# Optimization experiments

Hardware: AMD Instinct MI355X
Metric: run time of the kernel (lower is better)

Reference implementation:

```python
import jax, jax.numpy as jnp
import numpy as np

BS = 256          # batch size
N = 1000          # n_step_per_batch
ORDER = 2         # derivative order -> 3 vars (u, u', u'') per step
D = ORDER + 1
STEP_LOGIT = float(np.log(0.001 / 0.999))  # logit(0.001); sigmoid -> 0.001 step size


def mlp(x, w1, b1, w2, b2, w3, b3):
    h = jax.nn.relu(x @ w1 + b1)
    h = jax.nn.relu(h @ w2 + b2)
    return h @ w3 + b3


def build_A(c, h):
    # c: (N, 3) per-step equation coefficients; h: (N-1,) step sizes.
    # Rows: [1 initial-value] + [N equation] + [2*(N-1) Taylor smoothness (d=0,1)].
    R = 1 + N + 2 * (N - 1)
    i = jnp.arange(N)
    j = jnp.arange(N - 1)
    ones = jnp.ones(N - 1, c.dtype)
    rows = jnp.concatenate([
        jnp.array([0]),
        jnp.repeat(1 + i, 3),
        jnp.repeat(1 + N + 2 * j, 4),
        jnp.repeat(2 + N + 2 * j, 3)])
    cols = jnp.concatenate([
        jnp.array([0]),
        (i[:, None] * 3 + jnp.arange(3)).ravel(),
        jnp.stack([3 * j, 3 * j + 1, 3 * j + 2, 3 * (j + 1)], axis=1).ravel(),
        jnp.stack([3 * j + 1, 3 * j + 2, 3 * j + 4], axis=1).ravel()])
    vals = jnp.concatenate([
        jnp.ones(1, c.dtype),
        c.ravel(),
        jnp.stack([-ones, -h, -h * h / 2, ones], axis=1).ravel(),
        jnp.stack([-ones, -h, ones], axis=1).ravel()])
    return jnp.zeros((R, 3 * N), c.dtype).at[rows, cols].add(vals)


def ode_solve(coeffs, rhs, init_iv, steps):
    # coeffs (bs,1,N,3), rhs (bs,N,1), init_iv (bs,1), steps (bs,1,N-1)
    # coeffs/steps are batch-uniform in this model -> single shared system matrix.
    c = coeffs[0, 0]
    h = steps[0, 0]
    A = build_A(c, h)                       # (R, 3N)
    R = A.shape[0]
    b = jnp.zeros((R, BS), A.dtype)
    b = b.at[0].set(init_iv[:, 0]).at[1:1 + N].set(rhs[:, :, 0].T)
    AtA = A.T @ A + 1e-8 * jnp.eye(3 * N, dtype=A.dtype)
    u = jnp.linalg.solve(AtA, A.T @ b)      # (3N, BS) least-squares trajectory
    resid = A @ u - b
    eps = jnp.sqrt(jnp.sum(resid * resid, axis=0))  # (BS,) equation slack norm
    u = u.reshape(N, 3, BS)
    x0 = u[:, 0].T[:, :, None]              # (bs, N, 1)
    x1 = u[:, 1].T[:, :, None]
    x2 = u[:, 2].T[:, :, None]
    return x0, x1, x2, eps, steps


def reference(pin, ptime, pw1, pb1, pw2, pb2, pw3, pb3,
              tw1, tb1, tw2, tb2, tw3, tb3,
              nw1, nb1, nw2, nb2, nw3, nb3, net_iv):
    xi = mlp(pin, pw1, pb1, pw2, pb2, pw3, pb3).reshape(1, 3)
    ts = mlp(ptime, tw1, tb1, tw2, tb2, tw3, tb3).reshape(1, N)
    xi = jnp.tile(xi, (BS, 1))
    ts = jnp.tile(ts, (BS, 1))
    alpha = xi[:, 0:1][:, None, :]                 # (bs,1,1)
    beta = xi[:, 1:2][:, None, :]
    powr = jax.nn.sigmoid(xi[:, 2:3][:, None, :])
    ts = ts[:, None, :]                            # (bs,1,N)
    var = mlp(net_iv.reshape(BS, -1), nw1, nb1, nw2, nb2, nw3, nb3).reshape(BS, 1, N)
    rhs = jnp.abs(alpha * ts + beta * ts ** 2) ** powr * var ** 2 + ts
    rhs = jnp.transpose(rhs, (0, 2, 1))            # (bs, N, 1)
    coeffs = jnp.broadcast_to(jnp.array([0.0, 1.0, 0.0], net_iv.dtype), (BS, 1, N, 3))
    init_iv = var[:, :, 0]                         # (bs, 1)
    steps = jax.nn.sigmoid(jnp.full((BS, 1, N - 1), STEP_LOGIT, net_iv.dtype))
    x0, x1, x2, eps, steps = ode_solve(coeffs, rhs, init_iv, steps)
    x0 = jnp.transpose(x0, (0, 2, 1))              # (bs, 1, N)
    var = jnp.transpose(var, (0, 2, 1))            # (bs, N, 1)
    return (x0, steps, eps, var, ts[:, 0, :], alpha, beta, powr)


def setup_inputs() -> dict:
    key = jax.random.key(0)
    ks = jax.random.split(key, 24)
    f32 = jnp.float32

    def w(k, shape, scale=0.03):
        return (scale * jax.random.normal(k, shape)).astype(f32)

    inp = {
        "pin": w(ks[0], (1, 64), 1.0),
        "ptime": w(ks[1], (1, 64), 1.0),
        "pw1": w(ks[2], (64, 1024)), "pb1": jnp.zeros((1024,), f32),
        "pw2": w(ks[3], (1024, 1024)), "pb2": jnp.zeros((1024,), f32),
        "pw3": w(ks[4], (1024, 3)), "pb3": jnp.zeros((3,), f32),
        "tw1": w(ks[5], (64, 1024)), "tb1": jnp.zeros((1024,), f32),
        "tw2": w(ks[6], (1024, 1024)), "tb2": jnp.zeros((1024,), f32),
        "tw3": w(ks[7], (1024, N)), "tb3": jnp.zeros((N,), f32),
        "nw1": w(ks[8], (N, 1024)), "nb1": jnp.zeros((1024,), f32),
        "nw2": w(ks[9], (1024, 1024)), "nb2": jnp.zeros((1024,), f32),
        "nw3": w(ks[10], (1024, N)), "nb3": jnp.zeros((N,), f32),
        "net_iv": jax.random.normal(ks[11], (BS, N)).astype(f32),
    }
    return inp
```

## Files before the change

### kernel.cpp

```cpp
#include <hip/hip_runtime.h>
#include <math.h>

#define NN 1000
#define NIT 4
#define NKT 16

typedef _Float16 f16;
typedef _Float16 f16x8 __attribute__((ext_vector_type(8)));
typedef _Float16 f16x4 __attribute__((ext_vector_type(4)));
typedef float    f32x4 __attribute__((ext_vector_type(4)));

#define WS_H1P 0
#define WS_H1T 1024
#define WS_H2P 2048
#define WS_H2T 3072
#define WS_TS  4096
#define WS_XI  5120
#define WF_A0  540672
#define WF_H1  802816
#define WF_H2  1064960
#define WF_BT1 1327104
#define WF_BT2 2375680
#define WF_BT3 3424256

#define O_X0    0
#define O_STEP  256000
#define O_EPS   511744
#define O_VAR   512000
#define O_TS    768000
#define O_ALPHA 1024000
#define O_BETA  1024256
#define O_POWR  1024512

__device__ __forceinline__ void conv_bt_body(int idx, const float* __restrict__ W, int K0, int NW,
                                             f16* __restrict__ BT, float (*T)[32][33])
{
    const int tid = threadIdx.x;
    const int tx = tid & 31, ty = tid >> 5;
    const int kt = (idx & 31) * 32, ntile = (idx >> 5) * 32;
    #pragma unroll
    for (int i = 0; i < 4; ++i) {
        int k = kt + ty + i * 8, n = ntile + tx;
        (*T)[ty + i * 8][tx] = (k < K0 && n < NW) ? W[(size_t)k * NW + n] : 0.f;
    }
    __syncthreads();
    #pragma unroll
    for (int i = 0; i < 4; ++i) {
        int n = ntile + ty + i * 8, k = kt + tx;
        BT[(size_t)n * 1024 + k] = (f16)(*T)[tx][ty + i * 8];
    }
}

__device__ __forceinline__ void conv_a_body(int row, const float* __restrict__ in, f16* __restrict__ a0)
{
    const int t = threadIdx.x;
    float4 v = {0.f, 0.f, 0.f, 0.f};
    if (t < 250) v = ((const float4*)(in + row * 1000))[t];
    f16x4 h = {(f16)v.x, (f16)v.y, (f16)v.z, (f16)v.w};
    *(f16x4*)&a0[row * 1024 + t * 4] = h;
}

__device__ __forceinline__ void l1_body(int sub, const float* __restrict__ pin,
    const float* __restrict__ pw1, const float* __restrict__ pb1,
    const float* __restrict__ ptime, const float* __restrict__ tw1, const float* __restrict__ tb1,
    float* __restrict__ ws, float* sin_)
{
    const int tid = threadIdx.x;
    const bool tp = sub >= 4;
    const float* in = tp ? ptime : pin;
    const float* W  = tp ? tw1 : pw1;
    const float* B  = tp ? tb1 : pb1;
    float* outp = ws + (tp ? WS_H1T : WS_H1P);
    const int bxl = sub & 3;
    if (tid < 64) sin_[tid] = in[tid];
    __syncthreads();
    const int u = bxl * 256 + tid;
    float acc = B[u];
    #pragma unroll 16
    for (int k = 0; k < 64; ++k) acc += sin_[k] * W[k * 1024 + u];
    outp[u] = fmaxf(acc, 0.f);
}

__device__ __forceinline__ void l2_body(int lb, const float* __restrict__ pw2, const float* __restrict__ pb2,
    const float* __restrict__ tw2, const float* __restrict__ tb2, float* __restrict__ ws,
    float (*red)[16][17])
{
    const bool tp = lb >= 64;
    const float* h = ws + (tp ? WS_H1T : WS_H1P);
    const float* W = tp ? tw2 : pw2;
    const float* B = tp ? tb2 : pb2;
    float* outp = ws + (tp ? WS_H2T : WS_H2P);
    const int u0 = (lb & 63) * 16;
    const int tid = threadIdx.x, ul = tid & 15, kc = tid >> 4;
    const float* wp = W + u0 + ul;
    float acc = 0.f;
    const int kbase = kc * 64;
    #pragma unroll 8
    for (int k = 0; k < 64; ++k) acc += h[kbase + k] * wp[(size_t)(kbase + k) * 1024];
    (*red)[kc][ul] = acc; __syncthreads();
    for (int s = 8; s; s >>= 1) { if (kc < s) (*red)[kc][ul] += (*red)[kc + s][ul]; __syncthreads(); }
    if (tid < 16) outp[u0 + tid] = fmaxf((*red)[0][tid] + B[u0 + tid], 0.f);
}

__device__ __forceinline__ void l3_body(int lb, const float* __restrict__ pw3, const float* __restrict__ pb3,
    const float* __restrict__ tw3, const float* __restrict__ tb3,
    float* __restrict__ ws, float* __restrict__ out,
    float (*red)[16][17], float* redx)
{
    const int tid = threadIdx.x;
    if (lb == 64) {
        const float* h2p = ws + WS_H2P;
        float p[3] = {0.f, 0.f, 0.f};
        for (int k = tid; k < 1024; k += 256) {
            float h = h2p[k];
            p[0] += h * pw3[k * 3 + 0];
            p[1] += h * pw3[k * 3 + 1];
            p[2] += h * pw3[k * 3 + 2];
        }
        float xi[3];
        #pragma unroll
        for (int j = 0; j < 3; ++j) {
            redx[tid] = p[j]; __syncthreads();
            for (int s = 128; s > 0; s >>= 1) {
                if (tid < s) redx[tid] += redx[tid + s];
                __syncthreads();
            }
            xi[j] = redx[0] + pb3[j];
            __syncthreads();
        }
        float alpha = xi[0], beta = xi[1];
        float powr = 1.f / (1.f + expf(-xi[2]));
        if (tid == 0) { ws[WS_XI + 0] = alpha; ws[WS_XI + 1] = beta; ws[WS_XI + 2] = powr; }
        out[O_ALPHA + tid] = alpha;
        out[O_BETA  + tid] = beta;
        out[O_POWR  + tid] = powr;
    } else {
        const float* h = ws + WS_H2T;
        const int u0 = lb * 16;
        const int ul = tid & 15, kc = tid >> 4;
        const int u = u0 + ul;
        float acc = 0.f;
        const int kbase = kc * 64;
        if (u < NN) {
            #pragma unroll 8
            for (int k = 0; k < 64; ++k) acc += h[kbase + k] * tw3[(size_t)(kbase + k) * NN + u];
        }
        (*red)[kc][ul] = acc; __syncthreads();
        for (int s = 8; s; s >>= 1) { if (kc < s) (*red)[kc][ul] += (*red)[kc + s][ul]; __syncthreads(); }
        if (tid < 16 && u0 + tid < NN) ws[WS_TS + u0 + tid] = (*red)[0][tid] + tb3[u0 + tid];
    }
}

template<bool F16OUT>
__device__ __forceinline__ void gemm16_body(int bx, const f16* __restrict__ A, const f16* __restrict__ BT,
    const float* __restrict__ bias, int NW, f16* __restrict__ Cf16, float* __restrict__ Cf32, int ldc,
    f16 (*As)[32][72], f16 (*Bs)[32][72])
{
    const int tid = threadIdx.x;
    const int lane = tid & 63, wave = tid >> 6;
    const int wm = wave >> 1, wn = wave & 1;
    const int m0 = (bx >> 5) * 32, n0 = (bx & 31) * 32;
    const int srow = tid >> 3, sc = tid & 7;
    const float4* gA = (const float4*)(A  + (size_t)(m0 + srow) * 1024 + sc * 8);
    const float4* gB = (const float4*)(BT + (size_t)(n0 + srow) * 1024 + sc * 8);

    f32x4 acc = {0.f, 0.f, 0.f, 0.f};

    float4 ra = gA[0], rb = gB[0];
    *(float4*)&As[0][srow][sc * 8] = ra;
    *(float4*)&Bs[0][srow][sc * 8] = rb;
    ra = gA[8]; rb = gB[8];
    __syncthreads();

    const int arow = wm * 16 + (lane & 15);
    const int brow = wn * 16 + (lane & 15);
    const int kf = (lane >> 4) * 8;

    #pragma unroll 2
    for (int t = 0; t < NKT; ++t) {
        const int cur = t & 1;
        float4 ra2 = {}, rb2 = {};
        if (t + 2 < NKT) { ra2 = gA[(t + 2) * 8]; rb2 = gB[(t + 2) * 8]; }

        const f16x8 a0 = *(const f16x8*)&As[cur][arow][kf];
        const f16x8 b0 = *(const f16x8*)&Bs[cur][brow][kf];
        acc = __builtin_amdgcn_mfma_f32_16x16x32_f16(a0, b0, acc, 0, 0, 0);
        const f16x8 a1 = *(const f16x8*)&As[cur][arow][32 + kf];
        const f16x8 b1 = *(const f16x8*)&Bs[cur][brow][32 + kf];
        acc = __builtin_amdgcn_mfma_f32_16x16x32_f16(a1, b1, acc, 0, 0, 0);

        __syncthreads();
        if (t + 1 < NKT) {
            *(float4*)&As[cur ^ 1][srow][sc * 8] = ra;
            *(float4*)&Bs[cur ^ 1][srow][sc * 8] = rb;
        }
        ra = ra2; rb = rb2;
        __syncthreads();
    }

    const int col = n0 + wn * 16 + (lane & 15);
    const int row = m0 + wm * 16 + (lane >> 4) * 4;
    const float bs = (col < NW) ? bias[col] : 0.f;
    #pragma unroll
    for (int j = 0; j < 4; ++j) {
        float v = acc[j] + bs;
        if (F16OUT) {
            v = fmaxf(v, 0.f);
            Cf16[(size_t)(row + j) * 1024 + col] = (f16)v;
        } else if (col < NW) {
            Cf32[(size_t)(row + j) * ldc + col] = v;
        }
    }
}

__global__ __launch_bounds__(256) void k_s1(const float* __restrict__ nw1, const float* __restrict__ net_iv,
    const float* __restrict__ pin, const float* __restrict__ pw1, const float* __restrict__ pb1,
    const float* __restrict__ ptime, const float* __restrict__ tw1, const float* __restrict__ tb1,
    float* __restrict__ ws, f16* __restrict__ wsh)
{
    __shared__ float T[32][33];
    __shared__ float sin_[64];
    const int bx = blockIdx.x;
    if (bx < 1024) {
        conv_bt_body(bx, nw1, 1000, 1024, wsh + WF_BT1, &T);
    } else if (bx < 1280) {
        conv_a_body(bx - 1024, net_iv, wsh + WF_A0);
    } else {
        l1_body(bx - 1280, pin, pw1, pb1, ptime, tw1, tb1, ws, sin_);
    }
}

__global__ __launch_bounds__(256) void k_s2(const float* __restrict__ nw2, const float* __restrict__ nb1,
    const float* __restrict__ pw2, const float* __restrict__ pb2,
    const float* __restrict__ tw2, const float* __restrict__ tb2,
    float* __restrict__ ws, f16* __restrict__ wsh)
{
    __shared__ f16 As[2][32][72];
    __shared__ f16 Bs[2][32][72];
    __shared__ float T[32][33];
    __shared__ float red[16][17];
    const int bx = blockIdx.x;
    if (bx < 256) {
        gemm16_body<true>(bx, wsh + WF_A0, wsh + WF_BT1, nb1, 1024, wsh + WF_H1, nullptr, 0, As, Bs);
    } else if (bx < 1280) {
        conv_bt_body(bx - 256, nw2, 1024, 1024, wsh + WF_BT2, &T);
    } else {
        l2_body(bx - 1280, pw2, pb2, tw2, tb2, ws, &red);
    }
}

__global__ __launch_bounds__(256) void k_s3(const float* __restrict__ nw3, const float* __restrict__ nb2,
    const float* __restrict__ pw3, const float* __restrict__ pb3,
    const float* __restrict__ tw3, const float* __restrict__ tb3,
    float* __restrict__ ws, f16* __restrict__ wsh, float* __restrict__ out)
{
    __shared__ f16 As[2][32][72];
    __shared__ f16 Bs[2][32][72];
    __shared__ float T[32][33];
    __shared__ float red[16][17];
    __shared__ float redx[256];
    const int bx = blockIdx.x;
    if (bx < 256) {
        gemm16_body<true>(bx, wsh + WF_H1, wsh + WF_BT2, nb2, 1024, wsh + WF_H2, nullptr, 0, As, Bs);
    } else if (bx < 1280) {
        conv_bt_body(bx - 256, nw3, 1024, 1000, wsh + WF_BT3, &T);
    } else {
        l3_body(bx - 1280, pw3, pb3, tw3, tb3, ws, out, &red, redx);
    }
}

__global__ __launch_bounds__(256) void k_s4(const float* __restrict__ nb3,
    f16* __restrict__ wsh, float* __restrict__ out)
{
    __shared__ f16 As[2][32][72];
    __shared__ f16 Bs[2][32][72];
    gemm16_body<false>(blockIdx.x, wsh + WF_H2, wsh + WF_BT3, nb3, 1000,
                       nullptr, out + O_VAR, 1000, As, Bs);
}

__device__ inline void d_shift_left(const double a[4], double b4[4], double* sh, int tid, double pad)
{
    __syncthreads();
    sh[tid] = a[0];
    __syncthreads();
    b4[0] = a[1]; b4[1] = a[2]; b4[2] = a[3];
    b4[3] = (tid < 255) ? sh[tid + 1] : pad;
}
__device__ inline void d_scan_fwd(const double a[4], double incl[4], double* swt, int tid)
{
    double p0 = a[0], p1 = p0 + a[1], p2 = p1 + a[2], p3 = p2 + a[3];
    int lane = tid & 63, wid = tid >> 6;
    double w = p3;
    #pragma unroll
    for (int d = 1; d < 64; d <<= 1) {
        double t = __shfl_up(w, d, 64);
        if (lane >= d) w += t;
    }
    __syncthreads();
    if (lane == 63) swt[wid] = w;
    __syncthreads();
    double off = w - p3;
    #pragma unroll
    for (int q = 0; q < 3; ++q) if (q < wid) off += swt[q];
    incl[0] = p0 + off; incl[1] = p1 + off; incl[2] = p2 + off; incl[3] = p3 + off;
}
__device__ inline void d_scan_rev(const double a[4], double incl[4], double* swt, int tid)
{
    double s3 = a[3], s2 = s3 + a[2], s1 = s2 + a[1], s0 = s1 + a[0];
    int lane = tid & 63, wid = tid >> 6;
    double w = s0;
    #pragma unroll
    for (int d = 1; d < 64; d <<= 1) {
        double t = __shfl_down(w, d, 64);
        if (lane < 64 - d) w += t;
    }
    __syncthreads();
    if (lane == 0) swt[wid] = w;
    __syncthreads();
    double off = w - s0;
    #pragma unroll
    for (int q = 1; q < 4; ++q) if (q > wid) off += swt[q];
    incl[0] = s0 + off; incl[1] = s1 + off; incl[2] = s2 + off; incl[3] = s3 + off;
}

__global__ __launch_bounds__(256) void k_ode(const float* __restrict__ ws, float* __restrict__ out)
{
    const int b = blockIdx.x;
    const int tid = threadIdx.x;
    const double H = 0.001, H2c = 0.5e-6, INVH = 1000.0, EPSR = 1e-8;

    __shared__ double sh[257];
    __shared__ double swt[4];

    const float alpha = ws[WS_XI + 0], beta = ws[WS_XI + 1], powr = ws[WS_XI + 2];

    const float4 tsv = *(const float4*)&ws[WS_TS + tid * 4];
    const float* varp = out + O_VAR + (size_t)b * NN;
    float vaa[4];
    #pragma unroll
    for (int k = 0; k < 4; ++k) {
        int i = tid * 4 + k;
        vaa[k] = (i < NN) ? varp[i] : 0.f;
    }
    const double init = (double)varp[0];

    float tsa[4] = {tsv.x, tsv.y, tsv.z, tsv.w};

    double r[4];
    #pragma unroll
    for (int k = 0; k < 4; ++k) {
        int i = tid * 4 + k;
        float tf = tsa[k], vf = vaa[k];
        float basef = fabsf(alpha * tf + beta * tf * tf);
        float rr = powf(basef, powr) * vf * vf + tf;
        r[k] = (i < NN) ? (double)rr : 0.0;
    }

    double rn[4];
    d_shift_left(r, rn, sh, tid, 0.0);
    double ux[4], ud[4], us[4], g[4], gi[4];
    #pragma unroll
    for (int k = 0; k < 4; ++k) {
        int i = tid * 4 + k;
        ud[k] = r[k];
        us[k] = (i < NN - 1) ? (rn[k] - r[k]) * INVH : 0.0;
        g[k]  = (i < NN - 1) ? 0.5 * H * (r[k] + rn[k]) : 0.0;
    }
    d_scan_fwd(g, gi, swt, tid);
    #pragma unroll
    for (int k = 0; k < 4; ++k) {
        int i = tid * 4 + k;
        ux[k] = (i < NN) ? (init + (gi[k] - g[k])) : 0.0;
    }

    double tx[4] = {0,0,0,0}, td[4] = {0,0,0,0}, tss[4] = {0,0,0,0};
    for (int it = 0; it < NIT; ++it) {
        double a[4], yx0 = 0.0;
        #pragma unroll
        for (int k = 0; k < 4; ++k) {
            int i = tid * 4 + k;
            double yx = ux[k] - EPSR * tx[k];
            if (k == 0) yx0 = yx;
            a[k] = (i == 0) ? 0.0 : yx;
        }
        double S[4]; d_scan_rev(a, S, swt, tid);
        double wP[4];
        #pragma unroll
        for (int k = 0; k < 4; ++k) wP[k] = S[k] - a[k];
        double wV[4];
        #pragma unroll
        for (int k = 0; k < 4; ++k) {
            int i = tid * 4 + k;
            double ys = us[k] - EPSR * tss[k];
            wV[k] = (i < NN - 1) ? -(ys + H2c * wP[k]) * INVH : 0.0;
        }
        __syncthreads();
        sh[tid] = wV[3];
        if (tid == 0) sh[256] = yx0 + wP[0];
        __syncthreads();
        double wVm[4];
        wVm[1] = wV[0]; wVm[2] = wV[1]; wVm[3] = wV[2];
        wVm[0] = (tid > 0) ? sh[tid - 1] : 0.0;
        const double w0 = sh[256];

        double wD[4];
        #pragma unroll
        for (int k = 0; k < 4; ++k) {
            int i = tid * 4 + k;
            double yd = ud[k] - EPSR * td[k];
            wD[k] = (i < NN) ? (yd + ((i < NN - 1) ? H * wP[k] : 0.0) - wVm[k] + wV[k]) : 0.0;
        }
        double wDn[4]; d_shift_left(wD, wDn, sh, tid, 0.0);
        #pragma unroll
        for (int k = 0; k < 4; ++k) {
            int i = tid * 4 + k;
            td[k]  = wD[k];
            tss[k] = (i < NN - 1) ? (wDn[k] - wD[k] - wV[k]) * INVH : 0.0;
            g[k]   = (i < NN - 1) ? (H * td[k] + H2c * tss[k] + wP[k]) : 0.0;
        }
        d_scan_fwd(g, gi, swt, tid);
        #pragma unroll
        for (int k = 0; k < 4; ++k) {
            int i = tid * 4 + k;
            tx[k] = (i < NN) ? (w0 + (gi[k] - g[k])) : 0.0;
        }
    }

    double dx[4], dd[4], ds_[4];
    #pragma unroll
    for (int k = 0; k < 4; ++k) { dx[k] = -EPSR * tx[k]; dd[k] = -EPSR * td[k]; ds_[k] = -EPSR * tss[k]; }

    #pragma unroll
    for (int k = 0; k < 4; ++k) {
        int i = tid * 4 + k;
        if (i < NN) {
            out[O_X0  + b * NN + i] = (float)(ux[k] + dx[k]);
            out[O_TS  + b * NN + i] = tsa[k];
        }
        if (i < NN - 1) out[O_STEP + b * (NN - 1) + i] = 0.001f;
    }

    double dxn[4], ddn[4];
    d_shift_left(dx, dxn, sh, tid, 0.0);
    d_shift_left(dd, ddn, sh, tid, 0.0);
    double ss = 0.0;
    #pragma unroll
    for (int k = 0; k < 4; ++k) {
        int i = tid * 4 + k;
        if (i < NN) ss += dd[k] * dd[k];
        if (i == 0) ss += dx[k] * dx[k];
        if (i < NN - 1) {
            double rp = dxn[k] - dx[k] - H * dd[k] - H2c * ds_[k];
            double rv = ddn[k] - dd[k] - H * ds_[k];
            ss += rp * rp + rv * rv;
        }
    }
    const int lane = tid & 63, wid = tid >> 6;
    #pragma unroll
    for (int d = 32; d; d >>= 1) ss += __shfl_down(ss, d, 64);
    __syncthreads();
    if (lane == 0) swt[wid] = ss;
    __syncthreads();
    if (tid == 0) out[O_EPS + b] = (float)sqrt(swt[0] + swt[1] + swt[2] + swt[3]);
}

extern "C" void kernel_launch(void* const* d_in, const int* in_sizes, int n_in,
                              void* d_out, int out_size, void* d_ws, size_t ws_size,
                              hipStream_t stream)
{
    const float* pin    = (const float*)d_in[0];
    const float* ptime  = (const float*)d_in[1];
    const float* pw1    = (const float*)d_in[2];
    const float* pb1    = (const float*)d_in[3];
    const float* pw2    = (const float*)d_in[4];
    const float* pb2    = (const float*)d_in[5];
    const float* pw3    = (const float*)d_in[6];
    const float* pb3    = (const float*)d_in[7];
    const float* tw1    = (const float*)d_in[8];
    const float* tb1    = (const float*)d_in[9];
    const float* tw2    = (const float*)d_in[10];
    const float* tb2    = (const float*)d_in[11];
    const float* tw3    = (const float*)d_in[12];
    const float* tb3    = (const float*)d_in[13];
    const float* nw1    = (const float*)d_in[14];
    const float* nb1    = (const float*)d_in[15];
    const float* nw2    = (const float*)d_in[16];
    const float* nb2    = (const float*)d_in[17];
    const float* nw3    = (const float*)d_in[18];
    const float* nb3    = (const float*)d_in[19];
    const float* net_iv = (const float*)d_in[20];
    float* out = (float*)d_out;
    float* ws  = (float*)d_ws;
    f16*   wsh = (f16*)d_ws;

    k_s1 <<<1288, 256, 0, stream>>>(nw1, net_iv, pin, pw1, pb1, ptime, tw1, tb1, ws, wsh);
    k_s2 <<<1408, 256, 0, stream>>>(nw2, nb1, pw2, pb2, tw2, tb2, ws, wsh);
    k_s3 <<<1345, 256, 0, stream>>>(nw3, nb2, pw3, pb3, tw3, tb3, ws, wsh, out);
    k_s4 <<<256,  256, 0, stream>>>(nb3, wsh, out);
    k_ode<<<256,  256, 0, stream>>>(ws, out);
}
```

Before: 44.19 us.

## Halve ODE iterations, move constant output writes into GEMM kernel, merge shifts

Cuts the iteration count of the iterative solve in the ODE kernel from 4 to 2. The ts and step-size output writes move out of the ODE kernel into extra blocks of the final GEMM launch, so they run alongside the GEMM. The two back-to-back shared-memory shift passes are merged into one barrier pair by using a second shared buffer. Fewer iterations may lower solution accuracy if the iteration has not converged.

```diff
diff --git a/kernel.cpp b/kernel.cpp
--- a/kernel.cpp
+++ b/kernel.cpp
@@ -2,7 +2,7 @@
 #include <math.h>
 
 #define NN 1000
-#define NIT 4
+#define NIT 2
 #define NKT 16
 
 typedef _Float16 f16;
@@ -270,12 +270,24 @@
 }
 
 __global__ __launch_bounds__(256) void k_s4(const float* __restrict__ nb3,
-    f16* __restrict__ wsh, float* __restrict__ out)
+    const float* __restrict__ ws, f16* __restrict__ wsh, float* __restrict__ out)
 {
     __shared__ f16 As[2][32][72];
     __shared__ f16 Bs[2][32][72];
-    gemm16_body<false>(blockIdx.x, wsh + WF_H2, wsh + WF_BT3, nb3, 1000,
-                       nullptr, out + O_VAR, 1000, As, Bs);
+    const int bx = blockIdx.x;
+    if (bx < 256) {
+        gemm16_body<false>(bx, wsh + WF_H2, wsh + WF_BT3, nb3, 1000,
+                           nullptr, out + O_VAR, 1000, As, Bs);
+    } else {
+        const int b = bx - 256;
+        const int tid = threadIdx.x;
+        #pragma unroll
+        for (int k = 0; k < 4; ++k) {
+            int i = tid * 4 + k;
+            if (i < NN)     out[O_TS   + b * NN + i]       = ws[WS_TS + i];
+            if (i < NN - 1) out[O_STEP + b * (NN - 1) + i] = 0.001f;
+        }
+    }
 }
 
 __device__ inline void d_shift_left(const double a[4], double b4[4], double* sh, int tid, double pad)
@@ -330,6 +342,7 @@
     const double H = 0.001, H2c = 0.5e-6, INVH = 1000.0, EPSR = 1e-8;
 
     __shared__ double sh[257];
+    __shared__ double sh2[257];
     __shared__ double swt[4];
 
     const float alpha = ws[WS_XI + 0], beta = ws[WS_XI + 1], powr = ws[WS_XI + 2];
@@ -433,16 +446,18 @@
     #pragma unroll
     for (int k = 0; k < 4; ++k) {
         int i = tid * 4 + k;
-        if (i < NN) {
-            out[O_X0  + b * NN + i] = (float)(ux[k] + dx[k]);
-            out[O_TS  + b * NN + i] = tsa[k];
-        }
-        if (i < NN - 1) out[O_STEP + b * (NN - 1) + i] = 0.001f;
-    }
-
+        if (i < NN) out[O_X0 + b * NN + i] = (float)(ux[k] + dx[k]);
+    }
+
+    __syncthreads();
+    sh[tid] = dx[0]; sh2[tid] = dd[0];
+    __syncthreads();
     double dxn[4], ddn[4];
-    d_shift_left(dx, dxn, sh, tid, 0.0);
-    d_shift_left(dd, ddn, sh, tid, 0.0);
+    dxn[0] = dx[1]; dxn[1] = dx[2]; dxn[2] = dx[3];
+    dxn[3] = (tid < 255) ? sh[tid + 1] : 0.0;
+    ddn[0] = dd[1]; ddn[1] = dd[2]; ddn[2] = dd[3];
+    ddn[3] = (tid < 255) ? sh2[tid + 1] : 0.0;
+
     double ss = 0.0;
     #pragma unroll
     for (int k = 0; k < 4; ++k) {
@@ -496,6 +511,6 @@
     k_s1 <<<1288, 256, 0, stream>>>(nw1, net_iv, pin, pw1, pb1, ptime, tw1, tb1, ws, wsh);
     k_s2 <<<1408, 256, 0, stream>>>(nw2, nb1, pw2, pb2, tw2, tb2, ws, wsh);
     k_s3 <<<1345, 256, 0, stream>>>(nw3, nb2, pw3, pb3, tw3, tb3, ws, wsh, out);
-    k_s4 <<<256,  256, 0, stream>>>(nb3, wsh, out);
+    k_s4 <<<512,  256, 0, stream>>>(nb3, ws, wsh, out);
     k_ode<<<256,  256, 0, stream>>>(ws, out);
 }
```

Result: faster. 41.30 us (-6.5%).
